# Kernel tuning notes

Measured on AMD Instinct MI355X. Metric: run time of the kernel, lower is better.

Reference implementation:

```python
import jax, jax.numpy as jnp
import numpy as np

B, C, HH, WW = 16, 256, 64, 64
K, H, U, R = 16, 4, 4, 23
DIM_OUT = 256
DV = DIM_OUT // H  # 64
N = HH * WW
EPS = 1e-3  # keras BatchNormalization default epsilon


def setup_inputs() -> dict:
    key = jax.random.key(0)
    ks = jax.random.split(key, 16)
    sc = 0.02
    return {
        "x": jax.random.normal(ks[0], (B, C, HH, WW), jnp.float32),
        "w_q": jax.random.normal(ks[1], (K * H, C), jnp.float32) * sc,
        "w_k": jax.random.normal(ks[2], (K * U, C), jnp.float32) * sc,
        "w_v": jax.random.normal(ks[3], (DV * U, C), jnp.float32) * sc,
        "gamma_q": jnp.ones((K * H,), jnp.float32),
        "beta_q": jnp.zeros((K * H,), jnp.float32),
        "mean_q": jax.random.normal(ks[4], (K * H,), jnp.float32) * 0.1,
        "var_q": jax.random.uniform(ks[5], (K * H,), jnp.float32) + 0.5,
        "gamma_v": jnp.ones((DV * U,), jnp.float32),
        "beta_v": jnp.zeros((DV * U,), jnp.float32),
        "mean_v": jax.random.normal(ks[6], (DV * U,), jnp.float32) * 0.1,
        "var_v": jax.random.uniform(ks[7], (DV * U,), jnp.float32) + 0.5,
        "w_pos": jax.random.normal(ks[8], (K, U, 1, R, R), jnp.float32) * sc,
        "b_pos": jnp.zeros((K,), jnp.float32),
    }


def _bn(x, gamma, beta, mean, var):
    # inference-mode batchnorm over channel axis 1, x: [b,c,h,w]
    inv = gamma * jax.lax.rsqrt(var + EPS)
    return x * inv[None, :, None, None] + (beta - mean * inv)[None, :, None, None]


def reference(x, w_q, w_k, w_v, gamma_q, beta_q, mean_q, var_q,
              gamma_v, beta_v, mean_v, var_v, w_pos, b_pos):
    b = x.shape[0]
    # 1x1 conv projections (channels-first)
    q = jnp.einsum('oc,bchw->bohw', w_q, x)
    k = jnp.einsum('oc,bchw->bohw', w_k, x)
    v = jnp.einsum('oc,bchw->bohw', w_v, x)
    q = _bn(q, gamma_q, beta_q, mean_q, var_q)
    v = _bn(v, gamma_v, beta_v, mean_v, var_v)
    # rearrange to sequence form
    q = q.reshape(b, H, K, N)           # b h k n
    k = k.reshape(b, U, K, N)           # b u k m
    v = v.reshape(b, U, DV, N)          # b u v m
    k = jax.nn.softmax(k, axis=-1)      # softmax over positions m
    # content lambda
    Lc = jnp.einsum('bukm,buvm->bkv', k, v)
    Yc = jnp.einsum('bhkn,bkv->bnhv', q, Lc)
    # position lambda via local 3D conv over (v, hh, ww) with kernel (1, r, r)
    v5 = v.reshape(b, U, DV, HH, WW)
    Lp = jax.lax.conv_general_dilated(
        v5, w_pos, window_strides=(1, 1, 1),
        padding=[(0, 0), (R // 2, R // 2), (R // 2, R // 2)],
        dimension_numbers=('NCDHW', 'OIDHW', 'NCDHW'))
    Lp = Lp + b_pos[None, :, None, None, None]
    Lp = Lp.reshape(b, K, DV, N)        # b k v n
    Yp = jnp.einsum('bhkn,bkvn->bnhv', q, Lp)
    Y = Yc + Yp                          # [b, n, h, v]
    out = Y.transpose(0, 2, 3, 1).reshape(b, H * DV, HH, WW)
    return out
```

## Files before the change

### kernel.cpp

```cpp
#include <hip/hip_runtime.h>
#include <stdint.h>

#define EPS 1e-3f

typedef _Float16 f16x8 __attribute__((ext_vector_type(8)));
typedef float f32x4 __attribute__((ext_vector_type(4)));
typedef float f32x16 __attribute__((ext_vector_type(16)));

__global__ __launch_bounds__(256) void setup_kernel(
    const float* __restrict__ w_pos,
    const float* __restrict__ w_q, const float* __restrict__ w_k,
    const float* __restrict__ w_v,
    const float* __restrict__ gq, const float* __restrict__ bq,
    const float* __restrict__ mq, const float* __restrict__ vq,
    const float* __restrict__ gv, const float* __restrict__ bv,
    const float* __restrict__ mv, const float* __restrict__ vvar,
    float* __restrict__ scale_bias, float* __restrict__ Lc,
    float* __restrict__ Wt, _Float16* __restrict__ Apack) {
  const int idx = blockIdx.x * 256 + threadIdx.x;
  if (idx < 384) {
    float sc, bi;
    if (idx < 64) {
      const float inv = gq[idx] * rsqrtf(vq[idx] + EPS);
      sc = inv; bi = bq[idx] - mq[idx] * inv;
    } else if (idx < 128) {
      sc = 1.f; bi = 0.f;
    } else {
      const int o = idx - 128;
      const float inv = gv[o] * rsqrtf(vvar[o] + EPS);
      sc = inv; bi = bv[o] - mv[o] * inv;
    }
    scale_bias[idx] = sc;
    scale_bias[384 + idx] = bi;
  }
  if (idx < 16384) Lc[idx] = 0.f;
  if (idx < 98304) {
    const int row = idx % 384;
    const int k = idx / 384;
    float sc; const float* Wsrc;
    if (row < 64) {
      sc = gq[row] * rsqrtf(vq[row] + EPS);
      Wsrc = w_q + (size_t)row * 256;
    } else if (row < 128) {
      sc = 1.f;
      Wsrc = w_k + (size_t)(row - 64) * 256;
    } else {
      const int r = row - 128;
      sc = gv[r] * rsqrtf(vvar[r] + EPS);
      Wsrc = w_v + (size_t)r * 256;
    }
    Wt[idx] = Wsrc[k] * sc;
  }
  if (idx < 376832) {
    const int j = idx & 7;
    const int lane = (idx >> 3) & 63;
    const int f = idx >> 9;
    const int rel = f & 7;
    const int ss = (f >> 3) % 23;
    const int w = (f >> 3) / 23;
    const int m = lane & 31;
    const int kk = m & 15;
    const int ol = m >> 4;
    const int kap = lane >> 5;
    const int k = kap * 8 + j;
    const int u = k >> 2;
    const int y4 = k & 3;
    const int dy = 4 * rel + y4 - 2 * w - ol;
    float val = 0.f;
    if (dy >= 0 && dy < 23)
      val = w_pos[kk * 2116 + u * 529 + dy * 23 + ss];
    Apack[idx] = (_Float16)val;
  }
}

__global__ __launch_bounds__(256, 2) void proj_gemm(
    const float* __restrict__ x, const float* __restrict__ Wt,
    const float* __restrict__ scale_bias, float* __restrict__ proj) {
  const int b = blockIdx.y;
  const int nBase = blockIdx.x * 64;
  const int tid = threadIdx.x;
  const int tx = tid & 15, ty = tid >> 4;

  __shared__ float la[32][384];
  __shared__ float lb[32][64];

  float acc[6][4][4];
#pragma unroll
  for (int s = 0; s < 6; s++)
#pragma unroll
    for (int i = 0; i < 4; i++)
#pragma unroll
      for (int j = 0; j < 4; j++) acc[s][i][j] = 0.f;

  for (int k0 = 0; k0 < 256; k0 += 32) {
    __syncthreads();
    {
      const float4* src = (const float4*)&Wt[(size_t)k0 * 384];
      float4* dst = (float4*)&la[0][0];
#pragma unroll
      for (int r = 0; r < 12; ++r) dst[tid + r * 256] = src[tid + r * 256];
    }
#pragma unroll
    for (int r = 0; r < 2; ++r) {
      const int i = tid + r * 256;
      const int c = i >> 4, n4 = (i & 15) * 4;
      *(float4*)&lb[c][n4] =
          *(const float4*)&x[((size_t)(b * 256 + k0 + c)) * 4096 + nBase + n4];
    }
    __syncthreads();
    for (int kk = 0; kk < 32; ++kk) {
      const float4 bv = *(const float4*)&lb[kk][tx * 4];
      const float bb[4] = {bv.x, bv.y, bv.z, bv.w};
#pragma unroll
      for (int s = 0; s < 6; ++s) {
        const float4 av = *(const float4*)&la[kk][s * 64 + ty * 4];
        const float a[4] = {av.x, av.y, av.z, av.w};
#pragma unroll
        for (int i = 0; i < 4; i++)
#pragma unroll
          for (int j = 0; j < 4; j++)
            acc[s][i][j] = fmaf(a[i], bb[j], acc[s][i][j]);
      }
    }
  }

#pragma unroll
  for (int s = 0; s < 6; ++s) {
#pragma unroll
    for (int i = 0; i < 4; i++) {
      const int oG = s * 64 + ty * 4 + i;
      const float bi = scale_bias[384 + oG];
      float4 r;
      r.x = acc[s][i][0] + bi;
      r.y = acc[s][i][1] + bi;
      r.z = acc[s][i][2] + bi;
      r.w = acc[s][i][3] + bi;
      *(float4*)&proj[((size_t)(b * 384 + oG)) * 4096 + nBase + tx * 4] = r;
    }
  }
}

__global__ __launch_bounds__(256) void softmax_k(float* __restrict__ proj) {
  const int row = blockIdx.x;
  const int b = row >> 6, c = row & 63;
  float* p = proj + ((size_t)(b * 384 + 64 + c)) * 4096;
  const int tid = threadIdx.x;

  float4 v[4];
  float vmax = -3.4e38f;
#pragma unroll
  for (int i = 0; i < 4; i++) {
    v[i] = ((const float4*)p)[tid + i * 256];
    vmax = fmaxf(vmax, fmaxf(fmaxf(v[i].x, v[i].y), fmaxf(v[i].z, v[i].w)));
  }
#pragma unroll
  for (int off = 32; off > 0; off >>= 1) vmax = fmaxf(vmax, __shfl_xor(vmax, off));
  __shared__ float redm[4], reds[4];
  if ((tid & 63) == 0) redm[tid >> 6] = vmax;
  __syncthreads();
  vmax = fmaxf(fmaxf(redm[0], redm[1]), fmaxf(redm[2], redm[3]));

  float sum = 0.f;
#pragma unroll
  for (int i = 0; i < 4; i++) {
    v[i].x = expf(v[i].x - vmax); sum += v[i].x;
    v[i].y = expf(v[i].y - vmax); sum += v[i].y;
    v[i].z = expf(v[i].z - vmax); sum += v[i].z;
    v[i].w = expf(v[i].w - vmax); sum += v[i].w;
  }
#pragma unroll
  for (int off = 32; off > 0; off >>= 1) sum += __shfl_xor(sum, off);
  if ((tid & 63) == 0) reds[tid >> 6] = sum;
  __syncthreads();
  sum = reds[0] + reds[1] + reds[2] + reds[3];
  const float inv = 1.f / sum;
#pragma unroll
  for (int i = 0; i < 4; i++) {
    v[i].x *= inv; v[i].y *= inv; v[i].z *= inv; v[i].w *= inv;
    ((float4*)p)[tid + i * 256] = v[i];
  }
}

__global__ __launch_bounds__(256) void lc_kernel(const float* __restrict__ proj,
                                                 float* __restrict__ Lc) {
  const int mc = blockIdx.x, b = blockIdx.y;
  const int m0 = mc * 128;
  const int tid = threadIdx.x;
  const int kk = tid & 15;
  const int dvb = tid >> 4;

  __shared__ float kT[16][132];
  __shared__ float vT[64][132];

  float a0 = 0.f, a1 = 0.f, a2 = 0.f, a3 = 0.f;

  for (int u = 0; u < 4; ++u) {
    __syncthreads();
#pragma unroll
    for (int r = 0; r < 2; ++r) {
      const int i = tid + r * 256;
      const int row = i >> 5, c4 = (i & 31) * 4;
      *(float4*)&kT[row][c4] =
          *(const float4*)&proj[((size_t)(b * 384 + 64 + u * 16 + row)) * 4096 + m0 + c4];
    }
#pragma unroll
    for (int r = 0; r < 8; ++r) {
      const int i = tid + r * 256;
      const int row = i >> 5, c4 = (i & 31) * 4;
      *(float4*)&vT[row][c4] =
          *(const float4*)&proj[((size_t)(b * 384 + 128 + u * 64 + row)) * 4096 + m0 + c4];
    }
    __syncthreads();
#pragma unroll 4
    for (int m = 0; m < 128; ++m) {
      const float kv = kT[kk][m];
      a0 = fmaf(kv, vT[dvb * 4 + 0][m], a0);
      a1 = fmaf(kv, vT[dvb * 4 + 1][m], a1);
      a2 = fmaf(kv, vT[dvb * 4 + 2][m], a2);
      a3 = fmaf(kv, vT[dvb * 4 + 3][m], a3);
    }
  }

  float* dst = &Lc[((size_t)(b * 16 + kk)) * 64 + dvb * 4];
  atomicAdd(dst + 0, a0);
  atomicAdd(dst + 1, a1);
  atomicAdd(dst + 2, a2);
  atomicAdd(dst + 3, a3);
}

template <int W>
__device__ __forceinline__ void conv_worker(
    const _Float16* __restrict__ vL, const f16x8* __restrict__ Awl,
    const float* __restrict__ qsec, const float* __restrict__ lcb,
    const int n, const int kap, const int b, const int dv,
    float* __restrict__ out) {
  constexpr bool G0 = (W < 2);
  constexpr bool G6 = (W != 0);
  constexpr bool G7 = (W == 3);

  f16x8 A[8];
  if (G0) A[0] = Awl[0 * 64];
#pragma unroll
  for (int r = 1; r < 6; ++r) A[r] = Awl[r * 64];
  if (G6) A[6] = Awl[6 * 64];
  if (G7) A[7] = Awl[7 * 64];

#pragma unroll 1
  for (int pass = 0; pass < 2; ++pass) {
    f32x16 acc[8];
#pragma unroll
    for (int t = 0; t < 8; t++) acc[t] = (f32x16)0.f;

#pragma unroll 1
    for (int ss = 0; ss < 23; ++ss) {
      const int ssn = (ss == 22) ? 0 : ss + 1;
      const f16x8* Awn = Awl + (size_t)(ssn * 8) * 64;
      const _Float16* brow = &vL[(32 * pass + n + ss) * 360 + 8 * kap];

      f16x8 Bq[22];
      if (G0) Bq[0] = *(const f16x8*)__builtin_assume_aligned(brow, 16);
#pragma unroll
      for (int tau = 1; tau < 4; ++tau)
        Bq[tau] = *(const f16x8*)__builtin_assume_aligned(brow + 16 * tau, 16);

#pragma unroll
      for (int tau = 0; tau < 22; ++tau) {
        const int tpf = tau + 4;
        if (tpf < 22) {
          const bool live = (tpf == 20) ? G6 : (tpf == 21) ? G7 : true;
          if (live)
            Bq[tpf] = *(const f16x8*)__builtin_assume_aligned(brow + 16 * tpf, 16);
        }
        __builtin_amdgcn_s_setprio(1);
#pragma unroll
        for (int t = 0; t < 8; ++t) {
          const int rel = tau - 2 * t;
          if (rel < 0 || rel > 7) continue;
          if ((rel == 0 && !G0) || (rel == 6 && !G6) || (rel == 7 && !G7)) continue;
          acc[t] = __builtin_amdgcn_mfma_f32_32x32x16_f16(A[rel], Bq[tau], acc[t], 0, 0, 0);
        }
        __builtin_amdgcn_s_setprio(0);
        if (tau >= 14) {
          const int rn = tau - 14;
          const bool live = (rn == 0) ? G0 : (rn == 6) ? G6 : (rn == 7) ? G7 : true;
          if (live) A[rn] = Awn[rn * 64];
        }
      }
    }

    const int c = 32 * pass + n;
#pragma unroll 1
    for (int t = 0; t < 8; ++t) {
#pragma unroll
      for (int ol = 0; ol < 2; ++ol) {
        const int gamma = 8 * t + 2 * W + ol;
        const float* qg = qsec + (size_t)gamma * 64 + c;
        float y0 = 0.f, y1 = 0.f, y2 = 0.f, y3 = 0.f;
#pragma unroll
        for (int e = 0; e < 8; ++e) {
          const int kk = (e & 3) + 8 * (e >> 2) + 4 * kap;
          const float cf = acc[t][ol * 8 + e] + lcb[e];
          y0 = fmaf(qg[(size_t)(kk) * 4096], cf, y0);
          y1 = fmaf(qg[(size_t)(16 + kk) * 4096], cf, y1);
          y2 = fmaf(qg[(size_t)(32 + kk) * 4096], cf, y2);
          y3 = fmaf(qg[(size_t)(48 + kk) * 4096], cf, y3);
        }
        y0 += __shfl_xor(y0, 32);
        y1 += __shfl_xor(y1, 32);
        y2 += __shfl_xor(y2, 32);
        y3 += __shfl_xor(y3, 32);
        const float s0 = kap ? y2 : y0;
        const float s1 = kap ? y3 : y1;
        out[((size_t)(b * 256 + (2 * kap + 0) * 64 + dv)) * 4096 + gamma * 64 + c] = s0;
        out[((size_t)(b * 256 + (2 * kap + 1) * 64 + dv)) * 4096 + gamma * 64 + c] = s1;
      }
    }
  }
}

__global__ __launch_bounds__(256, 2) void lambda_conv(
    const float* __restrict__ proj, const _Float16* __restrict__ Apack,
    const float* __restrict__ Lc, const float* __restrict__ b_pos,
    float* __restrict__ out) {
  const int dv = blockIdx.x;
  const int b = blockIdx.y;
  const int tid = threadIdx.x;
  const int w = tid >> 6;
  const int lane = tid & 63;
  const int n = lane & 31;
  const int kap = lane >> 5;

  __shared__ __align__(16) _Float16 vL[86 * 360];

  {
    const uint4 z = {0u, 0u, 0u, 0u};
    for (int i = tid; i < (86 * 360 * 2) / 16; i += 256) ((uint4*)vL)[i] = z;
  }
  __syncthreads();

  {
    const float* vsec = proj + ((size_t)(b * 384 + 128 + dv)) * 4096;
    for (int idx = tid; idx < 4096; idx += 256) {
      const int u = idx >> 10, g = (idx >> 4) & 63, c4 = (idx & 15) * 4;
      const float4 vv = *(const float4*)&vsec[(size_t)u * 64 * 4096 + g * 64 + c4];
      const int sy = g + 11;
      const int qoff = (sy >> 2) * 16 + (u << 2) + (sy & 3);
      _Float16* base = &vL[(c4 + 11) * 360 + qoff];
      base[0 * 360] = (_Float16)vv.x;
      base[1 * 360] = (_Float16)vv.y;
      base[2 * 360] = (_Float16)vv.z;
      base[3 * 360] = (_Float16)vv.w;
    }
  }
  __syncthreads();

  float lcb[8];
#pragma unroll
  for (int e = 0; e < 8; e++) {
    const int kk = (e & 3) + 8 * (e >> 2) + 4 * kap;
    lcb[e] = Lc[(b * 16 + kk) * 64 + dv] + b_pos[kk];
  }

  const float* qsec = proj + ((size_t)(b * 384)) * 4096;
  const f16x8* Ap = (const f16x8*)Apack;
  const f16x8* Awl = Ap + (size_t)(w * 184) * 64 + lane;

  switch (w) {
    case 0: conv_worker<0>(vL, Awl, qsec, lcb, n, kap, b, dv, out); break;
    case 1: conv_worker<1>(vL, Awl, qsec, lcb, n, kap, b, dv, out); break;
    case 2: conv_worker<2>(vL, Awl, qsec, lcb, n, kap, b, dv, out); break;
    default: conv_worker<3>(vL, Awl, qsec, lcb, n, kap, b, dv, out); break;
  }
}

extern "C" void kernel_launch(void* const* d_in, const int* in_sizes, int n_in,
                              void* d_out, int out_size, void* d_ws, size_t ws_size,
                              hipStream_t stream) {
  const float* x       = (const float*)d_in[0];
  const float* w_q     = (const float*)d_in[1];
  const float* w_k     = (const float*)d_in[2];
  const float* w_v     = (const float*)d_in[3];
  const float* gamma_q = (const float*)d_in[4];
  const float* beta_q  = (const float*)d_in[5];
  const float* mean_q  = (const float*)d_in[6];
  const float* var_q   = (const float*)d_in[7];
  const float* gamma_v = (const float*)d_in[8];
  const float* beta_v  = (const float*)d_in[9];
  const float* mean_v  = (const float*)d_in[10];
  const float* var_v   = (const float*)d_in[11];
  const float* w_pos   = (const float*)d_in[12];
  const float* b_pos   = (const float*)d_in[13];

  float* ws = (float*)d_ws;
  float* proj = ws;
  float* sb   = ws + 25165824;
  float* Lc   = sb + 768;
  _Float16* Apack = (_Float16*)(Lc + 16384);
  float* Wt   = (float*)(Apack + 376832);
  float* out = (float*)d_out;

  setup_kernel<<<1472, 256, 0, stream>>>(w_pos, w_q, w_k, w_v,
                                         gamma_q, beta_q, mean_q, var_q,
                                         gamma_v, beta_v, mean_v, var_v,
                                         sb, Lc, Wt, Apack);
  proj_gemm<<<dim3(64, 16), 256, 0, stream>>>(x, Wt, sb, proj);
  softmax_k<<<1024, 256, 0, stream>>>(proj);
  lc_kernel<<<dim3(32, 16), 256, 0, stream>>>(proj, Lc);
  lambda_conv<<<dim3(64, 16), 256, 0, stream>>>(proj, Apack, Lc, b_pos, out);
}
```

Measured before the change: 619.6 us.

## Move projection GEMM to fp16 MFMA and split lambda conv across blocks

The fp32 FMA projection GEMM becomes an fp16 MFMA 32x32x16 kernel. Weights are pre-packed in fragment layout by the setup kernel and x is transposed into LDS as fp16. The lambda conv kernel is split so each block handles half the output tiles per dv, with a smaller LDS buffer reloaded per pass, which doubles the grid and raises the occupancy target to 3 blocks per CU. The fp16 inputs to the projection add precision loss relative to fp32 accumulation of fp32 inputs. Each conv block also redundantly reloads and reconverts v data.

```diff
diff --git a/kernel.cpp b/kernel.cpp
--- a/kernel.cpp
+++ b/kernel.cpp
@@ -6,6 +6,18 @@
 typedef _Float16 f16x8 __attribute__((ext_vector_type(8)));
 typedef float f32x4 __attribute__((ext_vector_type(4)));
 typedef float f32x16 __attribute__((ext_vector_type(16)));
+
+template <int W>
+constexpr bool rel_live(int rel) {
+  return !(rel < 0 || rel > 7 || (rel == 0 && W >= 2) ||
+           (rel == 6 && W == 0) || (rel == 7 && W != 3));
+}
+template <int W, int H>
+constexpr bool tau_live(int tau) {
+  for (int tt = 0; tt < 4; ++tt)
+    if (rel_live<W>(tau - 2 * (4 * H + tt))) return true;
+  return false;
+}
 
 __global__ __launch_bounds__(256) void setup_kernel(
     const float* __restrict__ w_pos,
@@ -16,7 +28,7 @@
     const float* __restrict__ gv, const float* __restrict__ bv,
     const float* __restrict__ mv, const float* __restrict__ vvar,
     float* __restrict__ scale_bias, float* __restrict__ Lc,
-    float* __restrict__ Wt, _Float16* __restrict__ Apack) {
+    _Float16* __restrict__ Wp, _Float16* __restrict__ Apack) {
   const int idx = blockIdx.x * 256 + threadIdx.x;
   if (idx < 384) {
     float sc, bi;
@@ -35,21 +47,26 @@
   }
   if (idx < 16384) Lc[idx] = 0.f;
   if (idx < 98304) {
-    const int row = idx % 384;
-    const int k = idx / 384;
+    const int j = idx & 7;
+    const int lane = (idx >> 3) & 63;
+    const int fr = idx >> 9;
+    const int kt = fr & 15;
+    const int mt = fr >> 4;
+    const int m = mt * 32 + (lane & 31);
+    const int k = kt * 16 + (lane >> 5) * 8 + j;
     float sc; const float* Wsrc;
-    if (row < 64) {
-      sc = gq[row] * rsqrtf(vq[row] + EPS);
-      Wsrc = w_q + (size_t)row * 256;
-    } else if (row < 128) {
+    if (m < 64) {
+      sc = gq[m] * rsqrtf(vq[m] + EPS);
+      Wsrc = w_q + (size_t)m * 256;
+    } else if (m < 128) {
       sc = 1.f;
-      Wsrc = w_k + (size_t)(row - 64) * 256;
+      Wsrc = w_k + (size_t)(m - 64) * 256;
     } else {
-      const int r = row - 128;
+      const int r = m - 128;
       sc = gv[r] * rsqrtf(vvar[r] + EPS);
       Wsrc = w_v + (size_t)r * 256;
     }
-    Wt[idx] = Wsrc[k] * sc;
+    Wp[idx] = (_Float16)(Wsrc[k] * sc);
   }
   if (idx < 376832) {
     const int j = idx & 7;
@@ -73,69 +90,54 @@
   }
 }
 
-__global__ __launch_bounds__(256, 2) void proj_gemm(
-    const float* __restrict__ x, const float* __restrict__ Wt,
+__global__ __launch_bounds__(256) void proj_gemm(
+    const float* __restrict__ x, const _Float16* __restrict__ Wp,
     const float* __restrict__ scale_bias, float* __restrict__ proj) {
   const int b = blockIdx.y;
-  const int nBase = blockIdx.x * 64;
+  const int n0 = blockIdx.x * 32;
   const int tid = threadIdx.x;
-  const int tx = tid & 15, ty = tid >> 4;
-
-  __shared__ float la[32][384];
-  __shared__ float lb[32][64];
-
-  float acc[6][4][4];
-#pragma unroll
-  for (int s = 0; s < 6; s++)
-#pragma unroll
-    for (int i = 0; i < 4; i++)
-#pragma unroll
-      for (int j = 0; j < 4; j++) acc[s][i][j] = 0.f;
-
-  for (int k0 = 0; k0 < 256; k0 += 32) {
-    __syncthreads();
-    {
-      const float4* src = (const float4*)&Wt[(size_t)k0 * 384];
-      float4* dst = (float4*)&la[0][0];
-#pragma unroll
-      for (int r = 0; r < 12; ++r) dst[tid + r * 256] = src[tid + r * 256];
-    }
-#pragma unroll
-    for (int r = 0; r < 2; ++r) {
-      const int i = tid + r * 256;
-      const int c = i >> 4, n4 = (i & 15) * 4;
-      *(float4*)&lb[c][n4] =
-          *(const float4*)&x[((size_t)(b * 256 + k0 + c)) * 4096 + nBase + n4];
-    }
-    __syncthreads();
-    for (int kk = 0; kk < 32; ++kk) {
-      const float4 bv = *(const float4*)&lb[kk][tx * 4];
-      const float bb[4] = {bv.x, bv.y, bv.z, bv.w};
-#pragma unroll
-      for (int s = 0; s < 6; ++s) {
-        const float4 av = *(const float4*)&la[kk][s * 64 + ty * 4];
-        const float a[4] = {av.x, av.y, av.z, av.w};
-#pragma unroll
-        for (int i = 0; i < 4; i++)
-#pragma unroll
-          for (int j = 0; j < 4; j++)
-            acc[s][i][j] = fmaf(a[i], bb[j], acc[s][i][j]);
-      }
-    }
-  }
-
-#pragma unroll
-  for (int s = 0; s < 6; ++s) {
-#pragma unroll
-    for (int i = 0; i < 4; i++) {
-      const int oG = s * 64 + ty * 4 + i;
-      const float bi = scale_bias[384 + oG];
-      float4 r;
-      r.x = acc[s][i][0] + bi;
-      r.y = acc[s][i][1] + bi;
-      r.z = acc[s][i][2] + bi;
-      r.w = acc[s][i][3] + bi;
-      *(float4*)&proj[((size_t)(b * 384 + oG)) * 4096 + nBase + tx * 4] = r;
+  const int w = tid >> 6, lane = tid & 63;
+  const int col = lane & 31, kap = lane >> 5;
+
+  __shared__ __align__(16) _Float16 xT[32][264];
+
+#pragma unroll
+  for (int r = 0; r < 8; ++r) {
+    const int i = tid + r * 256;
+    const int k = i >> 3, n4 = (i & 7) * 4;
+    const float4 xv = *(const float4*)&x[((size_t)(b * 256 + k)) * 4096 + n0 + n4];
+    xT[n4 + 0][k] = (_Float16)xv.x;
+    xT[n4 + 1][k] = (_Float16)xv.y;
+    xT[n4 + 2][k] = (_Float16)xv.z;
+    xT[n4 + 3][k] = (_Float16)xv.w;
+  }
+  __syncthreads();
+
+  f32x16 acc[3];
+#pragma unroll
+  for (int i = 0; i < 3; ++i) acc[i] = (f32x16)0.f;
+
+  const f16x8* Wf = (const f16x8*)Wp;
+#pragma unroll
+  for (int kt = 0; kt < 16; ++kt) {
+    const f16x8 B =
+        *(const f16x8*)__builtin_assume_aligned(&xT[col][kt * 16 + kap * 8], 16);
+#pragma unroll
+    for (int i = 0; i < 3; ++i) {
+      const f16x8 A = Wf[(size_t)(((w * 3 + i) * 16 + kt) * 64) + lane];
+      acc[i] = __builtin_amdgcn_mfma_f32_32x32x16_f16(A, B, acc[i], 0, 0, 0);
+    }
+  }
+
+#pragma unroll
+  for (int i = 0; i < 3; ++i) {
+    const int mt = w * 3 + i;
+#pragma unroll
+    for (int reg = 0; reg < 16; ++reg) {
+      const int row = (reg & 3) + 8 * (reg >> 2) + 4 * kap;
+      const int o = mt * 32 + row;
+      proj[((size_t)(b * 384 + o)) * 4096 + n0 + col] =
+          acc[i][reg] + scale_bias[384 + o];
     }
   }
 }
@@ -228,78 +230,101 @@
   atomicAdd(dst + 3, a3);
 }
 
-template <int W>
+template <int W, int H>
 __device__ __forceinline__ void conv_worker(
-    const _Float16* __restrict__ vL, const f16x8* __restrict__ Awl,
-    const float* __restrict__ qsec, const float* __restrict__ lcb,
-    const int n, const int kap, const int b, const int dv,
-    float* __restrict__ out) {
-  constexpr bool G0 = (W < 2);
-  constexpr bool G6 = (W != 0);
-  constexpr bool G7 = (W == 3);
+    _Float16* __restrict__ vL, const f16x8* __restrict__ Awl,
+    const float* __restrict__ vsec, const float* __restrict__ qsec,
+    const float* __restrict__ lcb, const int n, const int kap, const int tid,
+    const int b, const int dv, float* __restrict__ out) {
+  constexpr int TLO = 8 * H;
 
   f16x8 A[8];
-  if (G0) A[0] = Awl[0 * 64];
-#pragma unroll
-  for (int r = 1; r < 6; ++r) A[r] = Awl[r * 64];
-  if (G6) A[6] = Awl[6 * 64];
-  if (G7) A[7] = Awl[7 * 64];
+#pragma unroll
+  for (int r = 0; r < 8; ++r)
+    if (rel_live<W>(r)) A[r] = Awl[r * 64];
+
+  {
+    const uint4 z = {0u, 0u, 0u, 0u};
+    for (int i = tid; i < 2520; i += 256) ((uint4*)vL)[i] = z;
+  }
+  __syncthreads();
 
 #pragma unroll 1
   for (int pass = 0; pass < 2; ++pass) {
-    f32x16 acc[8];
-#pragma unroll
-    for (int t = 0; t < 8; t++) acc[t] = (f32x16)0.f;
+    if (pass) {
+      __syncthreads();
+      const uint4 z = {0u, 0u, 0u, 0u};
+      uint4* zp = (uint4*)(vL + 44 * 360);
+      for (int i = tid; i < 540; i += 256) zp[i] = z;
+    }
+    {
+      const int xlo = pass ? 20 : 0;
+      const int xhi = pass ? 64 : 44;
+      const int roff = pass ? -20 : 12;
+      for (int idx = tid; idx < 4096; idx += 256) {
+        const int u = idx >> 10, g = (idx >> 4) & 63, x4 = (idx & 15) * 4;
+        if (x4 >= xlo && x4 < xhi) {
+          const float4 vv = *(const float4*)&vsec[(size_t)u * 262144 + g * 64 + x4];
+          const int sy = g + 11;
+          const int qoff = (sy >> 2) * 16 + (u << 2) + (sy & 3);
+          _Float16* base = &vL[(x4 + roff) * 360 + qoff];
+          base[0] = (_Float16)vv.x;
+          base[360] = (_Float16)vv.y;
+          base[720] = (_Float16)vv.z;
+          base[1080] = (_Float16)vv.w;
+        }
+      }
+    }
+    __syncthreads();
+
+    f32x16 acc[4];
+#pragma unroll
+    for (int t = 0; t < 4; ++t) acc[t] = (f32x16)0.f;
 
 #pragma unroll 1
     for (int ss = 0; ss < 23; ++ss) {
       const int ssn = (ss == 22) ? 0 : ss + 1;
       const f16x8* Awn = Awl + (size_t)(ssn * 8) * 64;
-      const _Float16* brow = &vL[(32 * pass + n + ss) * 360 + 8 * kap];
+      const _Float16* brow = &vL[(n + ss + 1) * 360 + 8 * kap];
 
       f16x8 Bq[22];
-      if (G0) Bq[0] = *(const f16x8*)__builtin_assume_aligned(brow, 16);
-#pragma unroll
-      for (int tau = 1; tau < 4; ++tau)
-        Bq[tau] = *(const f16x8*)__builtin_assume_aligned(brow + 16 * tau, 16);
-
-#pragma unroll
-      for (int tau = 0; tau < 22; ++tau) {
+#pragma unroll
+      for (int i = 0; i < 4; ++i)
+        if (tau_live<W, H>(TLO + i))
+          Bq[TLO + i] =
+              *(const f16x8*)__builtin_assume_aligned(brow + 16 * (TLO + i), 16);
+
+#pragma unroll
+      for (int tau = TLO; tau < TLO + 14; ++tau) {
         const int tpf = tau + 4;
-        if (tpf < 22) {
-          const bool live = (tpf == 20) ? G6 : (tpf == 21) ? G7 : true;
-          if (live)
-            Bq[tpf] = *(const f16x8*)__builtin_assume_aligned(brow + 16 * tpf, 16);
-        }
+        if (tpf < TLO + 14 && tau_live<W, H>(tpf))
+          Bq[tpf] = *(const f16x8*)__builtin_assume_aligned(brow + 16 * tpf, 16);
         __builtin_amdgcn_s_setprio(1);
 #pragma unroll
-        for (int t = 0; t < 8; ++t) {
-          const int rel = tau - 2 * t;
-          if (rel < 0 || rel > 7) continue;
-          if ((rel == 0 && !G0) || (rel == 6 && !G6) || (rel == 7 && !G7)) continue;
-          acc[t] = __builtin_amdgcn_mfma_f32_32x32x16_f16(A[rel], Bq[tau], acc[t], 0, 0, 0);
+        for (int tt = 0; tt < 4; ++tt) {
+          const int rel = tau - 2 * (4 * H + tt);
+          if (rel >= 0 && rel <= 7 && rel_live<W>(rel))
+            acc[tt] = __builtin_amdgcn_mfma_f32_32x32x16_f16(A[rel], Bq[tau],
+                                                             acc[tt], 0, 0, 0);
         }
         __builtin_amdgcn_s_setprio(0);
-        if (tau >= 14) {
-          const int rn = tau - 14;
-          const bool live = (rn == 0) ? G0 : (rn == 6) ? G6 : (rn == 7) ? G7 : true;
-          if (live) A[rn] = Awn[rn * 64];
-        }
+        const int rn = tau - (TLO + 6);
+        if (rn >= 0 && rn < 8 && rel_live<W>(rn)) A[rn] = Awn[rn * 64];
       }
     }
 
     const int c = 32 * pass + n;
 #pragma unroll 1
-    for (int t = 0; t < 8; ++t) {
+    for (int tt = 0; tt < 4; ++tt) {
 #pragma unroll
       for (int ol = 0; ol < 2; ++ol) {
-        const int gamma = 8 * t + 2 * W + ol;
+        const int gamma = 32 * H + 8 * tt + 2 * W + ol;
         const float* qg = qsec + (size_t)gamma * 64 + c;
         float y0 = 0.f, y1 = 0.f, y2 = 0.f, y3 = 0.f;
 #pragma unroll
         for (int e = 0; e < 8; ++e) {
           const int kk = (e & 3) + 8 * (e >> 2) + 4 * kap;
-          const float cf = acc[t][ol * 8 + e] + lcb[e];
+          const float cf = acc[tt][ol * 8 + e] + lcb[e];
           y0 = fmaf(qg[(size_t)(kk) * 4096], cf, y0);
           y1 = fmaf(qg[(size_t)(16 + kk) * 4096], cf, y1);
           y2 = fmaf(qg[(size_t)(32 + kk) * 4096], cf, y2);
@@ -318,11 +343,12 @@
   }
 }
 
-__global__ __launch_bounds__(256, 2) void lambda_conv(
+__global__ __launch_bounds__(256, 3) void lambda_conv(
     const float* __restrict__ proj, const _Float16* __restrict__ Apack,
     const float* __restrict__ Lc, const float* __restrict__ b_pos,
     float* __restrict__ out) {
-  const int dv = blockIdx.x;
+  const int dv = blockIdx.x >> 1;
+  const int h = blockIdx.x & 1;
   const int b = blockIdx.y;
   const int tid = threadIdx.x;
   const int w = tid >> 6;
@@ -330,29 +356,10 @@
   const int n = lane & 31;
   const int kap = lane >> 5;
 
-  __shared__ __align__(16) _Float16 vL[86 * 360];
-
-  {
-    const uint4 z = {0u, 0u, 0u, 0u};
-    for (int i = tid; i < (86 * 360 * 2) / 16; i += 256) ((uint4*)vL)[i] = z;
-  }
-  __syncthreads();
-
-  {
-    const float* vsec = proj + ((size_t)(b * 384 + 128 + dv)) * 4096;
-    for (int idx = tid; idx < 4096; idx += 256) {
-      const int u = idx >> 10, g = (idx >> 4) & 63, c4 = (idx & 15) * 4;
-      const float4 vv = *(const float4*)&vsec[(size_t)u * 64 * 4096 + g * 64 + c4];
-      const int sy = g + 11;
-      const int qoff = (sy >> 2) * 16 + (u << 2) + (sy & 3);
-      _Float16* base = &vL[(c4 + 11) * 360 + qoff];
-      base[0 * 360] = (_Float16)vv.x;
-      base[1 * 360] = (_Float16)vv.y;
-      base[2 * 360] = (_Float16)vv.z;
-      base[3 * 360] = (_Float16)vv.w;
-    }
-  }
-  __syncthreads();
+  __shared__ __align__(16) _Float16 vL[56 * 360];
+
+  const float* vsec = proj + ((size_t)(b * 384 + 128 + dv)) * 4096;
+  const float* qsec = proj + ((size_t)(b * 384)) * 4096;
 
   float lcb[8];
 #pragma unroll
@@ -361,15 +368,18 @@
     lcb[e] = Lc[(b * 16 + kk) * 64 + dv] + b_pos[kk];
   }
 
-  const float* qsec = proj + ((size_t)(b * 384)) * 4096;
   const f16x8* Ap = (const f16x8*)Apack;
   const f16x8* Awl = Ap + (size_t)(w * 184) * 64 + lane;
 
-  switch (w) {
-    case 0: conv_worker<0>(vL, Awl, qsec, lcb, n, kap, b, dv, out); break;
-    case 1: conv_worker<1>(vL, Awl, qsec, lcb, n, kap, b, dv, out); break;
-    case 2: conv_worker<2>(vL, Awl, qsec, lcb, n, kap, b, dv, out); break;
-    default: conv_worker<3>(vL, Awl, qsec, lcb, n, kap, b, dv, out); break;
+  switch (w | (h << 2)) {
+    case 0: conv_worker<0, 0>(vL, Awl, vsec, qsec, lcb, n, kap, tid, b, dv, out); break;
+    case 1: conv_worker<1, 0>(vL, Awl, vsec, qsec, lcb, n, kap, tid, b, dv, out); break;
+    case 2: conv_worker<2, 0>(vL, Awl, vsec, qsec, lcb, n, kap, tid, b, dv, out); break;
+    case 3: conv_worker<3, 0>(vL, Awl, vsec, qsec, lcb, n, kap, tid, b, dv, out); break;
+    case 4: conv_worker<0, 1>(vL, Awl, vsec, qsec, lcb, n, kap, tid, b, dv, out); break;
+    case 5: conv_worker<1, 1>(vL, Awl, vsec, qsec, lcb, n, kap, tid, b, dv, out); break;
+    case 6: conv_worker<2, 1>(vL, Awl, vsec, qsec, lcb, n, kap, tid, b, dv, out); break;
+    default: conv_worker<3, 1>(vL, Awl, vsec, qsec, lcb, n, kap, tid, b, dv, out); break;
   }
 }
 
@@ -396,15 +406,15 @@
   float* sb   = ws + 25165824;
   float* Lc   = sb + 768;
   _Float16* Apack = (_Float16*)(Lc + 16384);
-  float* Wt   = (float*)(Apack + 376832);
+  _Float16* Wp = Apack + 376832;
   float* out = (float*)d_out;
 
   setup_kernel<<<1472, 256, 0, stream>>>(w_pos, w_q, w_k, w_v,
                                          gamma_q, beta_q, mean_q, var_q,
                                          gamma_v, beta_v, mean_v, var_v,
-                                         sb, Lc, Wt, Apack);
-  proj_gemm<<<dim3(64, 16), 256, 0, stream>>>(x, Wt, sb, proj);
+                                         sb, Lc, Wp, Apack);
+  proj_gemm<<<dim3(128, 16), 256, 0, stream>>>(x, Wp, sb, proj);
   softmax_k<<<1024, 256, 0, stream>>>(proj);
   lc_kernel<<<dim3(32, 16), 256, 0, stream>>>(proj, Lc);
-  lambda_conv<<<dim3(64, 16), 256, 0, stream>>>(proj, Apack, Lc, b_pos, out);
-}
+  lambda_conv<<<dim3(128, 16), 256, 0, stream>>>(proj, Apack, Lc, b_pos, out);
+}
```

Result: faster. 560.0 us (-9.6%).

## Rewrite projection GEMM with fp16 MFMA and stagger conv worker start offsets

Applied to the files above, without the earlier changes.

The fp32 FMA projection GEMM is replaced by an MFMA 32x32x16 fp16 kernel. Weights are prepacked in fp16 fragment layout during setup, and each block transposes a 32-column x tile into shared memory as fp16. The aim is to cut the cost of the 1x1 conv projections, which dominate FLOPs, at some loss of input precision. Separately, each conv worker wave begins its ss loop at a different rotated offset, likely to spread shared-memory or cache access across waves.

```diff
diff --git a/kernel.cpp b/kernel.cpp
--- a/kernel.cpp
+++ b/kernel.cpp
@@ -16,7 +16,7 @@
     const float* __restrict__ gv, const float* __restrict__ bv,
     const float* __restrict__ mv, const float* __restrict__ vvar,
     float* __restrict__ scale_bias, float* __restrict__ Lc,
-    float* __restrict__ Wt, _Float16* __restrict__ Apack) {
+    _Float16* __restrict__ Wp, _Float16* __restrict__ Apack) {
   const int idx = blockIdx.x * 256 + threadIdx.x;
   if (idx < 384) {
     float sc, bi;
@@ -35,21 +35,26 @@
   }
   if (idx < 16384) Lc[idx] = 0.f;
   if (idx < 98304) {
-    const int row = idx % 384;
-    const int k = idx / 384;
+    const int j = idx & 7;
+    const int lane = (idx >> 3) & 63;
+    const int fr = idx >> 9;
+    const int kt = fr & 15;
+    const int mt = fr >> 4;
+    const int m = mt * 32 + (lane & 31);
+    const int k = kt * 16 + (lane >> 5) * 8 + j;
     float sc; const float* Wsrc;
-    if (row < 64) {
-      sc = gq[row] * rsqrtf(vq[row] + EPS);
-      Wsrc = w_q + (size_t)row * 256;
-    } else if (row < 128) {
+    if (m < 64) {
+      sc = gq[m] * rsqrtf(vq[m] + EPS);
+      Wsrc = w_q + (size_t)m * 256;
+    } else if (m < 128) {
       sc = 1.f;
-      Wsrc = w_k + (size_t)(row - 64) * 256;
+      Wsrc = w_k + (size_t)(m - 64) * 256;
     } else {
-      const int r = row - 128;
+      const int r = m - 128;
       sc = gv[r] * rsqrtf(vvar[r] + EPS);
       Wsrc = w_v + (size_t)r * 256;
     }
-    Wt[idx] = Wsrc[k] * sc;
+    Wp[idx] = (_Float16)(Wsrc[k] * sc);
   }
   if (idx < 376832) {
     const int j = idx & 7;
@@ -73,69 +78,54 @@
   }
 }
 
-__global__ __launch_bounds__(256, 2) void proj_gemm(
-    const float* __restrict__ x, const float* __restrict__ Wt,
+__global__ __launch_bounds__(256) void proj_gemm(
+    const float* __restrict__ x, const _Float16* __restrict__ Wp,
     const float* __restrict__ scale_bias, float* __restrict__ proj) {
   const int b = blockIdx.y;
-  const int nBase = blockIdx.x * 64;
+  const int n0 = blockIdx.x * 32;
   const int tid = threadIdx.x;
-  const int tx = tid & 15, ty = tid >> 4;
-
-  __shared__ float la[32][384];
-  __shared__ float lb[32][64];
-
-  float acc[6][4][4];
-#pragma unroll
-  for (int s = 0; s < 6; s++)
-#pragma unroll
-    for (int i = 0; i < 4; i++)
-#pragma unroll
-      for (int j = 0; j < 4; j++) acc[s][i][j] = 0.f;
-
-  for (int k0 = 0; k0 < 256; k0 += 32) {
-    __syncthreads();
-    {
-      const float4* src = (const float4*)&Wt[(size_t)k0 * 384];
-      float4* dst = (float4*)&la[0][0];
-#pragma unroll
-      for (int r = 0; r < 12; ++r) dst[tid + r * 256] = src[tid + r * 256];
-    }
-#pragma unroll
-    for (int r = 0; r < 2; ++r) {
-      const int i = tid + r * 256;
-      const int c = i >> 4, n4 = (i & 15) * 4;
-      *(float4*)&lb[c][n4] =
-          *(const float4*)&x[((size_t)(b * 256 + k0 + c)) * 4096 + nBase + n4];
-    }
-    __syncthreads();
-    for (int kk = 0; kk < 32; ++kk) {
-      const float4 bv = *(const float4*)&lb[kk][tx * 4];
-      const float bb[4] = {bv.x, bv.y, bv.z, bv.w};
-#pragma unroll
-      for (int s = 0; s < 6; ++s) {
-        const float4 av = *(const float4*)&la[kk][s * 64 + ty * 4];
-        const float a[4] = {av.x, av.y, av.z, av.w};
-#pragma unroll
-        for (int i = 0; i < 4; i++)
-#pragma unroll
-          for (int j = 0; j < 4; j++)
-            acc[s][i][j] = fmaf(a[i], bb[j], acc[s][i][j]);
-      }
-    }
-  }
-
-#pragma unroll
-  for (int s = 0; s < 6; ++s) {
-#pragma unroll
-    for (int i = 0; i < 4; i++) {
-      const int oG = s * 64 + ty * 4 + i;
-      const float bi = scale_bias[384 + oG];
-      float4 r;
-      r.x = acc[s][i][0] + bi;
-      r.y = acc[s][i][1] + bi;
-      r.z = acc[s][i][2] + bi;
-      r.w = acc[s][i][3] + bi;
-      *(float4*)&proj[((size_t)(b * 384 + oG)) * 4096 + nBase + tx * 4] = r;
+  const int w = tid >> 6, lane = tid & 63;
+  const int col = lane & 31, kap = lane >> 5;
+
+  __shared__ __align__(16) _Float16 xT[32][264];
+
+#pragma unroll
+  for (int r = 0; r < 8; ++r) {
+    const int i = tid + r * 256;
+    const int k = i >> 3, n4 = (i & 7) * 4;
+    const float4 xv = *(const float4*)&x[((size_t)(b * 256 + k)) * 4096 + n0 + n4];
+    xT[n4 + 0][k] = (_Float16)xv.x;
+    xT[n4 + 1][k] = (_Float16)xv.y;
+    xT[n4 + 2][k] = (_Float16)xv.z;
+    xT[n4 + 3][k] = (_Float16)xv.w;
+  }
+  __syncthreads();
+
+  f32x16 acc[3];
+#pragma unroll
+  for (int i = 0; i < 3; ++i) acc[i] = (f32x16)0.f;
+
+  const f16x8* Wf = (const f16x8*)Wp;
+#pragma unroll
+  for (int kt = 0; kt < 16; ++kt) {
+    const f16x8 B =
+        *(const f16x8*)__builtin_assume_aligned(&xT[col][kt * 16 + kap * 8], 16);
+#pragma unroll
+    for (int i = 0; i < 3; ++i) {
+      const f16x8 A = Wf[(size_t)(((w * 3 + i) * 16 + kt) * 64) + lane];
+      acc[i] = __builtin_amdgcn_mfma_f32_32x32x16_f16(A, B, acc[i], 0, 0, 0);
+    }
+  }
+
+#pragma unroll
+  for (int i = 0; i < 3; ++i) {
+    const int mt = w * 3 + i;
+#pragma unroll
+    for (int reg = 0; reg < 16; ++reg) {
+      const int row = (reg & 3) + 8 * (reg >> 2) + 4 * kap;
+      const int o = mt * 32 + row;
+      proj[((size_t)(b * 384 + o)) * 4096 + n0 + col] =
+          acc[i][reg] + scale_bias[384 + o];
     }
   }
 }
@@ -237,13 +227,14 @@
   constexpr bool G0 = (W < 2);
   constexpr bool G6 = (W != 0);
   constexpr bool G7 = (W == 3);
+  constexpr int SBASE = 6 * W;
 
   f16x8 A[8];
-  if (G0) A[0] = Awl[0 * 64];
-#pragma unroll
-  for (int r = 1; r < 6; ++r) A[r] = Awl[r * 64];
-  if (G6) A[6] = Awl[6 * 64];
-  if (G7) A[7] = Awl[7 * 64];
+  if (G0) A[0] = Awl[SBASE * 8 * 64 + 0 * 64];
+#pragma unroll
+  for (int r = 1; r < 6; ++r) A[r] = Awl[SBASE * 8 * 64 + r * 64];
+  if (G6) A[6] = Awl[SBASE * 8 * 64 + 6 * 64];
+  if (G7) A[7] = Awl[SBASE * 8 * 64 + 7 * 64];
 
 #pragma unroll 1
   for (int pass = 0; pass < 2; ++pass) {
@@ -252,7 +243,9 @@
     for (int t = 0; t < 8; t++) acc[t] = (f32x16)0.f;
 
 #pragma unroll 1
-    for (int ss = 0; ss < 23; ++ss) {
+    for (int sit = 0; sit < 23; ++sit) {
+      const int ssr = sit + SBASE;
+      const int ss = (ssr < 23) ? ssr : ssr - 23;
       const int ssn = (ss == 22) ? 0 : ss + 1;
       const f16x8* Awn = Awl + (size_t)(ssn * 8) * 64;
       const _Float16* brow = &vL[(32 * pass + n + ss) * 360 + 8 * kap];
@@ -342,7 +335,7 @@
     const float* vsec = proj + ((size_t)(b * 384 + 128 + dv)) * 4096;
     for (int idx = tid; idx < 4096; idx += 256) {
       const int u = idx >> 10, g = (idx >> 4) & 63, c4 = (idx & 15) * 4;
-      const float4 vv = *(const float4*)&vsec[(size_t)u * 64 * 4096 + g * 64 + c4];
+      const float4 vv = *(const float4*)&vsec[(size_t)u * 262144 + g * 64 + c4];
       const int sy = g + 11;
       const int qoff = (sy >> 2) * 16 + (u << 2) + (sy & 3);
       _Float16* base = &vL[(c4 + 11) * 360 + qoff];
@@ -396,14 +389,14 @@
   float* sb   = ws + 25165824;
   float* Lc   = sb + 768;
   _Float16* Apack = (_Float16*)(Lc + 16384);
-  float* Wt   = (float*)(Apack + 376832);
+  _Float16* Wp = Apack + 376832;
   float* out = (float*)d_out;
 
   setup_kernel<<<1472, 256, 0, stream>>>(w_pos, w_q, w_k, w_v,
                                          gamma_q, beta_q, mean_q, var_q,
                                          gamma_v, beta_v, mean_v, var_v,
-                                         sb, Lc, Wt, Apack);
-  proj_gemm<<<dim3(64, 16), 256, 0, stream>>>(x, Wt, sb, proj);
+                                         sb, Lc, Wp, Apack);
+  proj_gemm<<<dim3(128, 16), 256, 0, stream>>>(x, Wp, sb, proj);
   softmax_k<<<1024, 256, 0, stream>>>(proj);
   lc_kernel<<<dim3(32, 16), 256, 0, stream>>>(proj, Lc);
   lambda_conv<<<dim3(64, 16), 256, 0, stream>>>(proj, Apack, Lc, b_pos, out);
```

Result: faster. 534.4 us (-13.7%).
